# Optimization experiments

Hardware: AMD Instinct MI355X
Metric: run time of the kernel (lower is better)

## Reference

```python
import jax, jax.numpy as jnp
import numpy as np

MAX_LEN, BATCH, EMB = 512, 32, 41
HID, UNITS = 800, 20
BOND_LENS = jnp.array([1.329, 1.459, 1.525], jnp.float32)
BOND_ANGLES = jnp.array([2.034, 2.119, 1.937], jnp.float32)
INIT_ABC = jnp.array([[0.0, 0.0, 1.0], [0.0, 1.0, 0.0], [1.0, 0.0, 0.0]], jnp.float32)


def _lstm_dir(x, w_ih, w_hh, b, reverse):
    # x: [T, B, in]; returns hidden states [T, B, H]
    T, B, _ = x.shape
    H = w_hh.shape[1]
    xs = jnp.flip(x, 0) if reverse else x
    xw = jnp.einsum('tbi,gi->tbg', xs, w_ih) + b  # precompute input projection

    def step(carry, xt):
        h, c = carry
        gates = xt + h @ w_hh.T
        i, f, g, o = jnp.split(gates, 4, axis=-1)
        c = jax.nn.sigmoid(f) * c + jax.nn.sigmoid(i) * jnp.tanh(g)
        h = jax.nn.sigmoid(o) * jnp.tanh(c)
        return (h, c), h

    init = (jnp.zeros((B, H), x.dtype), jnp.zeros((B, H), x.dtype))
    _, hs = jax.lax.scan(step, init, xw)
    return jnp.flip(hs, 0) if reverse else hs


def _bilstm_layer(x, w_ih, w_hh, b):
    # w_ih: [2, 4H, in]; w_hh: [2, 4H, H]; b: [2, 4H]
    fwd = _lstm_dir(x, w_ih[0], w_hh[0], b[0], False)
    bwd = _lstm_dir(x, w_ih[1], w_hh[1], b[1], True)
    return jnp.concatenate([fwd, bwd], axis=-1)


def _geometric_unit(coords3, triplet):
    # coords3: [3, B, 3] last three atoms; triplet: [B, 3] torsion angles
    A, Bc, C = coords3[0], coords3[1], coords3[2]
    new = []
    for i in range(3):
        Tang, R, P = BOND_ANGLES[i], BOND_LENS[i], triplet[:, i]
        D2 = jnp.stack([-R * jnp.cos(Tang) * jnp.ones_like(P),
                        R * jnp.cos(P) * jnp.sin(Tang),
                        R * jnp.sin(P) * jnp.sin(Tang)], axis=1)  # [B,3]
        BC = C - Bc
        bc = BC / jnp.linalg.norm(BC, axis=1, keepdims=True)
        AB = Bc - A
        N = jnp.cross(AB, bc)
        n = N / jnp.linalg.norm(N, axis=1, keepdims=True)
        M = jnp.stack([bc, jnp.cross(n, bc), n], axis=2)  # [B,3,3]
        D = jnp.einsum('bij,bj->bi', M, D2) + C
        A, Bc, C = Bc, C, D
        new.append(D)
    return jnp.stack([A, Bc, C]), jnp.stack(new)  # carry, [3,B,3]


def setup_inputs() -> dict:
    key = jax.random.key(0)
    ks = jax.random.split(key, 10)
    k = 1.0 / np.sqrt(HID)
    u = lambda kk, shp, lim: jax.random.uniform(kk, shp, jnp.float32, -lim, lim)
    in0, in1 = EMB + 1, 2 * HID
    return {
        'sequences': jax.random.normal(ks[0], (MAX_LEN, BATCH, EMB), jnp.float32),
        'lengths': jnp.full((BATCH,), MAX_LEN, jnp.int64 if jax.config.jax_enable_x64 else jnp.int32),
        'w_ih0': u(ks[1], (2, 4 * HID, in0), k),
        'w_hh0': u(ks[2], (2, 4 * HID, HID), k),
        'b0': u(ks[3], (2, 4 * HID), k),
        'w_ih1': u(ks[4], (2, 4 * HID, in1), k),
        'w_hh1': u(ks[5], (2, 4 * HID, HID), k),
        'b1': u(ks[6], (2, 4 * HID), k),
        'lin_w': u(ks[7], (UNITS, 2 * HID), 1.0 / np.sqrt(2 * HID)),
        'lin_b': u(ks[8], (UNITS,), 1.0 / np.sqrt(2 * HID)),
        'alphabet': jax.random.uniform(ks[9], (UNITS, 3), jnp.float32, -3.14, 3.14),
    }


def reference(sequences, lengths, w_ih0, w_hh0, b0, w_ih1, w_hh1, b1, lin_w, lin_b, alphabet):
    T, B, _ = sequences.shape
    abs_pos = jnp.broadcast_to(jnp.arange(T, dtype=sequences.dtype)[:, None, None], (T, B, 1))
    x = jnp.concatenate([sequences, abs_pos], axis=2)  # [T, B, EMB+1]
    # 2-layer bidirectional LSTM (all lengths == max_len -> packing is identity)
    h = _bilstm_layer(x, w_ih0, w_hh0, b0)
    h = _bilstm_layer(h, w_ih1, w_hh1, b1)  # [T, B, 2H]
    # linear -> softmax over alphabet, trig angle decode
    soft = jax.nn.softmax(h @ lin_w.T + lin_b, axis=2)  # [T, B, UNITS]
    sine = soft @ jnp.sin(alphabet)   # [T, B, 3]
    cosine = soft @ jnp.cos(alphabet)
    out = jnp.arctan2(sine, cosine)   # torsion angle triplets
    # sequential geometric coordinate recurrence over timesteps 1..T-1
    init = jnp.broadcast_to(INIT_ABC[:, None, :], (3, B, 3))
    _, new_coords = jax.lax.scan(_geometric_unit, init, out[1:])  # [T-1, 3, B, 3]
    pred_coords = jnp.concatenate([init, new_coords.reshape(-1, B, 3)], axis=0)
    return pred_coords  # [3 + 3*(T-1), B, 3]
```

## Files before the change

kernel.cpp:

```cpp
#include <hip/hip_runtime.h>
#include <math.h>

#define T_LEN 512
#define NB    32
#define EMB_  41
#define IN0_  42
#define HID_  800
#define G4_   3200
#define IN1_  1600
#define NU    20
#define NCH   100

typedef unsigned short u16;
typedef unsigned int   u32;
typedef unsigned long long u64;
typedef __attribute__((ext_vector_type(8))) short short8;
typedef __attribute__((ext_vector_type(4))) float f32x4;

__device__ __forceinline__ float bf2f(u16 v) {
    union { u32 u; float f; } c; c.u = ((u32)v) << 16; return c.f;
}
__device__ __forceinline__ u16 f2bf(float f) {
    union { float f; u32 u; } c; c.f = f;
    u32 r = (c.u + 0x7fffu + ((c.u >> 16) & 1u)) >> 16;
    return (u16)r;
}
__device__ __forceinline__ short cvt_hl(float v, int hl) {
    u16 hi = f2bf(v);
    return hl ? (short)f2bf(v - bf2f(hi)) : (short)hi;
}
__device__ __forceinline__ f32x4 mfma16(short8 a, short8 b, f32x4 c) {
    return __builtin_amdgcn_mfma_f32_16x16x32_bf16(a, b, c, 0, 0, 0);
}
__device__ __forceinline__ void astore(u64* p, u64 v) {
    __hip_atomic_store(p, v, __ATOMIC_RELAXED, __HIP_MEMORY_SCOPE_AGENT);
}
__device__ __forceinline__ int afload(const int* p) {
    return __hip_atomic_load(p, __ATOMIC_RELAXED, __HIP_MEMORY_SCOPE_AGENT);
}
__device__ __forceinline__ void afstore(int* p, int v) {
    __hip_atomic_store(p, v, __ATOMIC_RELAXED, __HIP_MEMORY_SCOPE_AGENT);
}


__global__ __launch_bounds__(256, 1)
void lstm0_persist(const float* __restrict__ seq, const float* __restrict__ wih0,
                   const float* __restrict__ whh0, const float* __restrict__ bias,
                   u16* __restrict__ h0f, int* __restrict__ flags)
{
    __shared__ __align__(16) float part[2048];
    __shared__ __align__(16) u16 stageB[25600];
    __shared__ __align__(16) float w0l[32*48];
    __shared__ __align__(16) float xsl[32*48];
    __shared__ u16 hpk[NB*8];
    const int tid = threadIdx.x;
    const int d = blockIdx.x / NCH, ch = blockIdx.x % NCH;
    const int w = tid >> 6, l = tid & 63;
    const int p = w & 1, hl = w >> 1;
    int* myflags = flags + d*128;

    short8 wreg[25];
    {
        const int m = l & 15, g = p*2 + (m>>3), j = ch*8 + (m&7);
        const float* base = whh0 + ((size_t)(d*G4_ + g*HID_ + j))*HID_ + (l>>4)*8;
#pragma unroll
        for (int kc = 0; kc < 25; ++kc) {
            float4 f0 = *(const float4*)(base + kc*32);
            float4 f1 = *(const float4*)(base + kc*32 + 4);
            short8 v;
            v[0]=cvt_hl(f0.x,hl); v[1]=cvt_hl(f0.y,hl); v[2]=cvt_hl(f0.z,hl); v[3]=cvt_hl(f0.w,hl);
            v[4]=cvt_hl(f1.x,hl); v[5]=cvt_hl(f1.y,hl); v[6]=cvt_hl(f1.z,hl); v[7]=cvt_hl(f1.w,hl);
            wreg[kc] = v;
        }
    }
    for (int idx = tid; idx < 32*EMB_; idx += 256) {
        int r = idx / EMB_, k = idx % EMB_;
        int ju_ = r >> 2, g = r & 3;
        w0l[r*48 + k] = wih0[((size_t)(d*G4_ + g*HID_ + ch*8 + ju_))*IN0_ + k];
    }
    const int ju = tid >> 5, b = tid & 31;
    const int j = ch*8 + ju;
    const int nt = b >> 4, n = b & 15;
    float biasr[4], wpos[4];
#pragma unroll
    for (int g = 0; g < 4; ++g) {
        biasr[g] = bias[d*G4_ + g*HID_ + j];
        wpos[g]  = wih0[((size_t)(d*G4_ + g*HID_ + j))*IN0_ + EMB_];
    }
    float creg = 0.f;
    __syncthreads();

    for (int s = 0; s < T_LEN; ++s) {
        const int t = d ? (T_LEN-1-s) : s;

        for (int idx = tid; idx < 32*EMB_; idx += 256)
            xsl[(idx/EMB_)*48 + idx%EMB_] = seq[(size_t)t*(NB*EMB_) + idx];

        if (s > 0 && tid < NCH)
            while (afload(myflags + tid) < s) __builtin_amdgcn_s_sleep(1);
        __syncthreads();

        if (s == 0) {
#pragma unroll
            for (int q = 0; q < 25; ++q) ((u64*)stageB)[tid + q*256] = 0ull;
        } else {
            const int tprev = d ? (T_LEN - s) : (s - 1);
            const u64* src = (const u64*)(h0f + (size_t)tprev*51200) + d*6400;
            u64 tmp[25];
#pragma unroll
            for (int q = 0; q < 25; ++q) tmp[q] = src[tid + q*256];
#pragma unroll
            for (int q = 0; q < 25; ++q) ((u64*)stageB)[tid + q*256] = tmp[q];
        }
        __syncthreads();

        f32x4 acc0 = {0.f,0.f,0.f,0.f}, acc1 = {0.f,0.f,0.f,0.f};
#pragma unroll 5
        for (int kc = 0; kc < 25; ++kc) {
            short8 b0 = *(const short8*)(stageB + kc*1024 + l*8);
            short8 b1 = *(const short8*)(stageB + kc*1024 + 512 + l*8);
            acc0 = mfma16(wreg[kc], b0, acc0);
            acc1 = mfma16(wreg[kc], b1, acc1);
        }
        {
            const int mrow = (l>>4)*4, nn = l & 15;
#pragma unroll
            for (int r = 0; r < 4; ++r) {
                part[(((p*2+hl)*2 + 0)*16 + mrow + r)*16 + nn] = acc0[r];
                part[(((p*2+hl)*2 + 1)*16 + mrow + r)*16 + nn] = acc1[r];
            }
        }
        __syncthreads();

        float dot0 = 0.f, dot1 = 0.f, dot2 = 0.f, dot3 = 0.f;
        {
            const float* wr = &w0l[ju*4*48];
            const float* xr = &xsl[b*48];
#pragma unroll
            for (int k4 = 0; k4 < 40; k4 += 4) {
                float4 xk = *(const float4*)(xr + k4);
                float4 w0 = *(const float4*)(wr + 0*48 + k4);
                float4 w1 = *(const float4*)(wr + 1*48 + k4);
                float4 w2 = *(const float4*)(wr + 2*48 + k4);
                float4 w3 = *(const float4*)(wr + 3*48 + k4);
                dot0 += w0.x*xk.x + w0.y*xk.y + w0.z*xk.z + w0.w*xk.w;
                dot1 += w1.x*xk.x + w1.y*xk.y + w1.z*xk.z + w1.w*xk.w;
                dot2 += w2.x*xk.x + w2.y*xk.y + w2.z*xk.z + w2.w*xk.w;
                dot3 += w3.x*xk.x + w3.y*xk.y + w3.z*xk.z + w3.w*xk.w;
            }
            float xk = xr[40];
            dot0 += wr[0*48+40]*xk; dot1 += wr[1*48+40]*xk;
            dot2 += wr[2*48+40]*xk; dot3 += wr[3*48+40]*xk;
        }
        float v[4] = {dot0, dot1, dot2, dot3};
#pragma unroll
        for (int g = 0; g < 4; ++g) {
            const int pp = g >> 1, m = (g & 1)*8 + ju;
            v[g] += part[(((pp*2+0)*2 + nt)*16 + m)*16 + n]
                  + part[(((pp*2+1)*2 + nt)*16 + m)*16 + n]
                  + biasr[g] + (float)t * wpos[g];
        }
        float ig = 1.f/(1.f + expf(-v[0]));
        float fg = 1.f/(1.f + expf(-v[1]));
        float gg = tanhf(v[2]);
        float og = 1.f/(1.f + expf(-v[3]));
        creg = fg * creg + ig * gg;
        hpk[b*8 + ju] = f2bf(og * tanhf(creg));
        __syncthreads();

        if (tid < 64) {
            const int bb = tid >> 1, half = tid & 1;
            const u16* hp = &hpk[bb*8 + half*4];
            u64 pk = (u64)hp[0] | ((u64)hp[1]<<16) | ((u64)hp[2]<<32) | ((u64)hp[3]<<48);
            const int ntb = bb >> 4, llb = ((ch&3)<<4) | (bb&15);
            const int xoff = ((d*25 + (ch>>2))*2 + ntb)*128 + llb*2 + half;
            astore((u64*)(h0f + (size_t)t*51200) + xoff, pk);
        }
        __syncthreads();
        if (tid == 0) afstore(myflags + ch, s+1);
    }
}

__global__ __launch_bounds__(256, 1)
void lstm1_persist(const float* __restrict__ wih1, const float* __restrict__ whh1,
                   const float* __restrict__ bias, const float* __restrict__ lin_w,
                   const u16* __restrict__ h0f, u16* __restrict__ h1f,
                   int* __restrict__ flags, float* __restrict__ logits)
{
    __shared__ __align__(16) u16 wihL[2*50*512];
    __shared__ __align__(16) u16 stageB[25600];
    __shared__ __align__(16) float part[2048];
    __shared__ u16 hpk[NB*8];
    const int tid = threadIdx.x;
    const int d = blockIdx.x / NCH, ch = blockIdx.x % NCH;
    const int w = tid >> 6, l = tid & 63;
    const int p = w & 1, hl = w >> 1;
    int* myflags = flags + d*128;

    short8 wreg[25];
    {
        const int m = l & 15, g = p*2 + (m>>3), j = ch*8 + (m&7);
        const float* base = whh1 + ((size_t)(d*G4_ + g*HID_ + j))*HID_ + (l>>4)*8;
#pragma unroll
        for (int kc = 0; kc < 25; ++kc) {
            float4 f0 = *(const float4*)(base + kc*32);
            float4 f1 = *(const float4*)(base + kc*32 + 4);
            short8 v;
            v[0]=cvt_hl(f0.x,hl); v[1]=cvt_hl(f0.y,hl); v[2]=cvt_hl(f0.z,hl); v[3]=cvt_hl(f0.w,hl);
            v[4]=cvt_hl(f1.x,hl); v[5]=cvt_hl(f1.y,hl); v[6]=cvt_hl(f1.z,hl); v[7]=cvt_hl(f1.w,hl);
            wreg[kc] = v;
        }
    }
    for (int o = tid; o < 6400; o += 256) {
        int pp = o / 3200, r = o % 3200, kc = r >> 6, ll = r & 63;
        int m = ll & 15, g = pp*2 + (m>>3), jj = ch*8 + (m&7);
        const float* base = wih1 + ((size_t)(d*G4_ + g*HID_ + jj))*IN1_ + kc*32 + (ll>>4)*8;
        float4 f0 = *(const float4*)base;
        float4 f1 = *(const float4*)(base + 4);
        short8 v;
        v[0]=(short)f2bf(f0.x); v[1]=(short)f2bf(f0.y); v[2]=(short)f2bf(f0.z); v[3]=(short)f2bf(f0.w);
        v[4]=(short)f2bf(f1.x); v[5]=(short)f2bf(f1.y); v[6]=(short)f2bf(f1.z); v[7]=(short)f2bf(f1.w);
        *(short8*)&wihL[o*8] = v;
    }
    const int ol = tid >> 5, ln = tid & 31;
    const int lo = ch*7 + ol;
    const bool lown = (ol < 7) && (lo < NB*NU);
    int lofs = 0;
    float wlin[25];
    if (lown) {
        const int bb = lo / NU, uu = lo % NU;
        lofs = (bb >> 4)*512 + ((((ln >> 3) << 4) | (bb & 15)))*8 + (ln & 7);
        const float* wrow = lin_w + (size_t)uu*IN1_ + d*HID_ + ln;
#pragma unroll
        for (int i = 0; i < 25; ++i) wlin[i] = wrow[i*32];
    }
    const int ju = tid >> 5, b = tid & 31;
    const int j = ch*8 + ju;
    const int nt = b >> 4, n = b & 15;
    float biasr[4];
#pragma unroll
    for (int g = 0; g < 4; ++g) biasr[g] = bias[d*G4_ + g*HID_ + j];
    float creg = 0.f;
    __syncthreads();

    for (int s = 0; s < T_LEN; ++s) {
        const int t = d ? (T_LEN-1-s) : s;

        f32x4 acc0 = {0.f,0.f,0.f,0.f}, acc1 = {0.f,0.f,0.f,0.f};
        {
            const u16* xb = h0f + (size_t)t*51200;
#pragma unroll 5
            for (int kc = 0; kc < 25; ++kc) {
                const int idx = hl*25 + kc;
                short8 a  = *(const short8*)&wihL[(p*50 + idx)*512 + l*8];
                short8 b0 = *(const short8*)(xb + idx*1024 + l*8);
                short8 b1 = *(const short8*)(xb + idx*1024 + 512 + l*8);
                acc0 = mfma16(a, b0, acc0);
                acc1 = mfma16(a, b1, acc1);
            }
        }

        if (s > 0 && tid < NCH)
            while (afload(myflags + tid) < s) __builtin_amdgcn_s_sleep(1);
        __syncthreads();

        if (s == 0) {
#pragma unroll
            for (int q = 0; q < 25; ++q) ((u64*)stageB)[tid + q*256] = 0ull;
        } else {
            const int tprev = d ? (T_LEN - s) : (s - 1);
            const u64* src = (const u64*)(h1f + (size_t)tprev*51200) + d*6400;
            u64 tmp[25];
#pragma unroll
            for (int q = 0; q < 25; ++q) tmp[q] = src[tid + q*256];
#pragma unroll
            for (int q = 0; q < 25; ++q) ((u64*)stageB)[tid + q*256] = tmp[q];
        }
        __syncthreads();

#pragma unroll 5
        for (int kc = 0; kc < 25; ++kc) {
            short8 b0 = *(const short8*)(stageB + kc*1024 + l*8);
            short8 b1 = *(const short8*)(stageB + kc*1024 + 512 + l*8);
            acc0 = mfma16(wreg[kc], b0, acc0);
            acc1 = mfma16(wreg[kc], b1, acc1);
        }
        {
            const int mrow = (l>>4)*4, nn = l & 15;
#pragma unroll
            for (int r = 0; r < 4; ++r) {
                part[(((p*2+hl)*2 + 0)*16 + mrow + r)*16 + nn] = acc0[r];
                part[(((p*2+hl)*2 + 1)*16 + mrow + r)*16 + nn] = acc1[r];
            }
        }
        __syncthreads();

        float v[4];
#pragma unroll
        for (int g = 0; g < 4; ++g) {
            const int pp = g >> 1, m = (g & 1)*8 + ju;
            v[g] = part[(((pp*2+0)*2 + nt)*16 + m)*16 + n]
                 + part[(((pp*2+1)*2 + nt)*16 + m)*16 + n] + biasr[g];
        }
        float ig = 1.f/(1.f + expf(-v[0]));
        float fg = 1.f/(1.f + expf(-v[1]));
        float gg = tanhf(v[2]);
        float og = 1.f/(1.f + expf(-v[3]));
        creg = fg * creg + ig * gg;
        float hn = og * tanhf(creg);
        hpk[b*8 + ju] = f2bf(hn);
        __syncthreads();

        if (tid < 64) {
            const int bb = tid >> 1, half = tid & 1;
            const u16* hp = &hpk[bb*8 + half*4];
            u64 pk = (u64)hp[0] | ((u64)hp[1]<<16) | ((u64)hp[2]<<32) | ((u64)hp[3]<<48);
            const int ntb = bb >> 4, llb = ((ch&3)<<4) | (bb&15);
            const int xoff = ((d*25 + (ch>>2))*2 + ntb)*128 + llb*2 + half;
            astore((u64*)(h1f + (size_t)t*51200) + xoff, pk);
        }
        __syncthreads();
        if (tid == 0) afstore(myflags + ch, s+1);

        if (s > 0 && lown) {
            float sum = 0.f;
#pragma unroll
            for (int i = 0; i < 25; ++i)
                sum += bf2f(stageB[i*1024 + lofs]) * wlin[i];
#pragma unroll
            for (int off2 = 16; off2; off2 >>= 1) sum += __shfl_down(sum, off2, 32);
            if (ln == 0) {
                const int tprev = d ? (T_LEN - s) : (s - 1);
                logits[((size_t)d*T_LEN + tprev)*640 + lo] = sum;
            }
        }
    }
    if (tid < NCH)
        while (afload(myflags + tid) < T_LEN) __builtin_amdgcn_s_sleep(1);
    __syncthreads();
    {
        const int tlast = d ? 0 : (T_LEN - 1);
        const u64* src = (const u64*)(h1f + (size_t)tlast*51200) + d*6400;
        u64 tmp[25];
#pragma unroll
        for (int q = 0; q < 25; ++q) tmp[q] = src[tid + q*256];
#pragma unroll
        for (int q = 0; q < 25; ++q) ((u64*)stageB)[tid + q*256] = tmp[q];
    }
    __syncthreads();
    if (lown) {
        float sum = 0.f;
#pragma unroll
        for (int i = 0; i < 25; ++i)
            sum += bf2f(stageB[i*1024 + lofs]) * wlin[i];
#pragma unroll
        for (int off2 = 16; off2; off2 >>= 1) sum += __shfl_down(sum, off2, 32);
        if (ln == 0) {
            const int tprev = d ? 0 : (T_LEN - 1);
            logits[((size_t)d*T_LEN + tprev)*640 + lo] = sum;
        }
    }
}

__global__ __launch_bounds__(256)
void epilogue(const float* __restrict__ logits, const float* __restrict__ lin_b,
              const float* __restrict__ alphabet, float* __restrict__ cs)
{
    __shared__ float sa[NU*3], ca[NU*3], lb[NU];
    const int tid = threadIdx.x;
    if (tid < NU*3) { float al = alphabet[tid]; sa[tid] = sinf(al); ca[tid] = cosf(al); }
    if (tid < NU) lb[tid] = lin_b[tid];
    __syncthreads();
    const int row = blockIdx.x*256 + tid;
    if (row >= T_LEN*NB) return;
    const int t = row >> 5, b = row & 31;
    float lg[NU];
    float m = -1e30f;
#pragma unroll 4
    for (int u = 0; u < NU; ++u) {
        lg[u] = lb[u] + logits[(size_t)t*640 + b*NU + u]
                      + logits[((size_t)T_LEN + t)*640 + b*NU + u];
        m = fmaxf(m, lg[u]);
    }
    float ssum = 0.f;
#pragma unroll 4
    for (int u = 0; u < NU; ++u) { lg[u] = expf(lg[u] - m); ssum += lg[u]; }
    float inv = 1.f / ssum;
#pragma unroll
    for (int i = 0; i < 3; ++i) {
        float sv = 0.f, cv = 0.f;
#pragma unroll 4
        for (int u = 0; u < NU; ++u) {
            float sw = lg[u] * inv;
            sv += sw * sa[u*3 + i];
            cv += sw * ca[u*3 + i];
        }
        float rinv = rsqrtf(fmaxf(sv*sv + cv*cv, 1e-30f));
        *(float2*)(cs + ((size_t)row*3 + i)*2) = make_float2(cv*rinv, sv*rinv);
    }
}

__global__ __launch_bounds__(64)
void geometry(const float* __restrict__ cs, float* __restrict__ out)
{
    const int b = threadIdx.x;
    if (b >= NB) return;
    const float blen[3] = {1.329f, 1.459f, 1.525f};
    const float bang[3] = {2.034f, 2.119f, 1.937f};
    float sT[3], cT[3];
#pragma unroll
    for (int i = 0; i < 3; ++i) { sT[i] = sinf(bang[i]); cT[i] = cosf(bang[i]); }

    float Ax=0.f,Ay=0.f,Az=1.f, Bx=0.f,By=1.f,Bz=0.f, Cx=1.f,Cy=0.f,Cz=0.f;
    out[(0*NB + b)*3 + 0] = 0.f; out[(0*NB + b)*3 + 1] = 0.f; out[(0*NB + b)*3 + 2] = 1.f;
    out[(1*NB + b)*3 + 0] = 0.f; out[(1*NB + b)*3 + 1] = 1.f; out[(1*NB + b)*3 + 2] = 0.f;
    out[(2*NB + b)*3 + 0] = 1.f; out[(2*NB + b)*3 + 1] = 0.f; out[(2*NB + b)*3 + 2] = 0.f;

    for (int t = 1; t < T_LEN; ++t) {
        float2 pc[3];
#pragma unroll
        for (int i = 0; i < 3; ++i)
            pc[i] = *(const float2*)(cs + (((size_t)t*NB + b)*3 + i)*2);
#pragma unroll
        for (int i = 0; i < 3; ++i) {
            float R = blen[i];
            float d2x = -R*cT[i], d2y = R*pc[i].x*sT[i], d2z = R*pc[i].y*sT[i];
            float bcx = Cx-Bx, bcy = Cy-By, bcz = Cz-Bz;
            float inv = rsqrtf(bcx*bcx + bcy*bcy + bcz*bcz);
            bcx *= inv; bcy *= inv; bcz *= inv;
            float abx = Bx-Ax, aby = By-Ay, abz = Bz-Az;
            float nx = aby*bcz - abz*bcy;
            float ny = abz*bcx - abx*bcz;
            float nz = abx*bcy - aby*bcx;
            inv = rsqrtf(fmaxf(nx*nx + ny*ny + nz*nz, 1e-30f));
            nx *= inv; ny *= inv; nz *= inv;
            float mx = ny*bcz - nz*bcy;
            float my = nz*bcx - nx*bcz;
            float mz = nx*bcy - ny*bcx;
            float Dx = bcx*d2x + mx*d2y + nx*d2z + Cx;
            float Dy = bcy*d2x + my*d2y + ny*d2z + Cy;
            float Dz = bcz*d2x + mz*d2y + nz*d2z + Cz;
            Ax=Bx; Ay=By; Az=Bz; Bx=Cx; By=Cy; Bz=Cz; Cx=Dx; Cy=Dy; Cz=Dz;
            const int r = 3 + (t-1)*3 + i;
            out[((size_t)r*NB + b)*3 + 0] = Dx;
            out[((size_t)r*NB + b)*3 + 1] = Dy;
            out[((size_t)r*NB + b)*3 + 2] = Dz;
        }
    }
}

extern "C" void kernel_launch(void* const* d_in, const int* in_sizes, int n_in,
                              void* d_out, int out_size, void* d_ws, size_t ws_size,
                              hipStream_t stream)
{
    (void)in_sizes; (void)n_in; (void)out_size; (void)ws_size;
    const float* seq   = (const float*)d_in[0];
    const float* w_ih0 = (const float*)d_in[2];
    const float* w_hh0 = (const float*)d_in[3];
    const float* b0    = (const float*)d_in[4];
    const float* w_ih1 = (const float*)d_in[5];
    const float* w_hh1 = (const float*)d_in[6];
    const float* b1    = (const float*)d_in[7];
    const float* lin_w = (const float*)d_in[8];
    const float* lin_b = (const float*)d_in[9];
    const float* alpha = (const float*)d_in[10];

    char* ws = (char*)d_ws;
    size_t off = 0;
    u16* h0f   = (u16*)(ws + off); off += 52428800ull;
    u16* h1f   = (u16*)(ws + off); off += 52428800ull;
    int* flagsL0 = (int*)(ws + off); off += 1024ull;
    int* flagsL1 = (int*)(ws + off); off += 1024ull;
    float* logits = (float*)(ws + off); off += 2621440ull;
    float* cs = (float*)(ws + off); off += 393216ull;

    hipMemsetAsync(flagsL0, 0, 2048, stream);

    lstm0_persist<<<dim3(2*NCH), dim3(256), 0, stream>>>(seq, w_ih0, w_hh0, b0, h0f, flagsL0);

    lstm1_persist<<<dim3(2*NCH), dim3(256), 0, stream>>>(w_ih1, w_hh1, b1, lin_w, h0f, h1f,
                                                         flagsL1, logits);

    epilogue<<<dim3(64), dim3(256), 0, stream>>>(logits, lin_b, alpha, cs);
    geometry<<<dim3(1), dim3(64), 0, stream>>>(cs, (float*)d_out);
}
```

Before: 9.387 ms.

## Read hidden state directly from global memory and cut per-step barriers in persistent LSTMs

Each wave now polls the cross-block step flags itself with a wave-wide vote, instead of one thread group spinning followed by a block barrier. The hidden-state vector is loaded straight from global memory into the MFMA operands, no longer staged through LDS with an extra barrier. The flag store is issued by wave 0 after a vmcnt wait rather than after a block-wide barrier, and the input slice buffer is double-buffered to avoid a write-after-read hazard. This shortens the serial critical path of each timestep, at the cost of redundant global and L2 reads per wave and weaker ordering guarantees on the relaxed atomics.

```diff
diff --git a/kernel.cpp b/kernel.cpp
--- a/kernel.cpp
+++ b/kernel.cpp
@@ -49,9 +49,8 @@
                    u16* __restrict__ h0f, int* __restrict__ flags)
 {
     __shared__ __align__(16) float part[2048];
-    __shared__ __align__(16) u16 stageB[25600];
     __shared__ __align__(16) float w0l[32*48];
-    __shared__ __align__(16) float xsl[32*48];
+    __shared__ __align__(16) float xsl[2][32*48];
     __shared__ u16 hpk[NB*8];
     const int tid = threadIdx.x;
     const int d = blockIdx.x / NCH, ch = blockIdx.x % NCH;
@@ -88,39 +87,34 @@
         wpos[g]  = wih0[((size_t)(d*G4_ + g*HID_ + j))*IN0_ + EMB_];
     }
     float creg = 0.f;
+    const int pi1 = l, pi2 = (l + 64 < NCH) ? (l + 64) : l;
     __syncthreads();
 
     for (int s = 0; s < T_LEN; ++s) {
         const int t = d ? (T_LEN-1-s) : s;
 
         for (int idx = tid; idx < 32*EMB_; idx += 256)
-            xsl[(idx/EMB_)*48 + idx%EMB_] = seq[(size_t)t*(NB*EMB_) + idx];
-
-        if (s > 0 && tid < NCH)
-            while (afload(myflags + tid) < s) __builtin_amdgcn_s_sleep(1);
-        __syncthreads();
-
-        if (s == 0) {
-#pragma unroll
-            for (int q = 0; q < 25; ++q) ((u64*)stageB)[tid + q*256] = 0ull;
-        } else {
+            xsl[s&1][(idx/EMB_)*48 + idx%EMB_] = seq[(size_t)t*(NB*EMB_) + idx];
+
+        if (s > 0) {
+            for (;;) {
+                bool ok = (afload(myflags + pi1) >= s) && (afload(myflags + pi2) >= s);
+                if (__all(ok)) break;
+                __builtin_amdgcn_s_sleep(1);
+            }
+        }
+
+        f32x4 acc0 = {0.f,0.f,0.f,0.f}, acc1 = {0.f,0.f,0.f,0.f};
+        if (s > 0) {
             const int tprev = d ? (T_LEN - s) : (s - 1);
-            const u64* src = (const u64*)(h0f + (size_t)tprev*51200) + d*6400;
-            u64 tmp[25];
-#pragma unroll
-            for (int q = 0; q < 25; ++q) tmp[q] = src[tid + q*256];
-#pragma unroll
-            for (int q = 0; q < 25; ++q) ((u64*)stageB)[tid + q*256] = tmp[q];
-        }
-        __syncthreads();
-
-        f32x4 acc0 = {0.f,0.f,0.f,0.f}, acc1 = {0.f,0.f,0.f,0.f};
+            const u16* hb = h0f + (size_t)tprev*51200 + d*25600;
 #pragma unroll 5
-        for (int kc = 0; kc < 25; ++kc) {
-            short8 b0 = *(const short8*)(stageB + kc*1024 + l*8);
-            short8 b1 = *(const short8*)(stageB + kc*1024 + 512 + l*8);
-            acc0 = mfma16(wreg[kc], b0, acc0);
-            acc1 = mfma16(wreg[kc], b1, acc1);
+            for (int kc = 0; kc < 25; ++kc) {
+                short8 b0 = *(const short8*)(hb + kc*1024 + l*8);
+                short8 b1 = *(const short8*)(hb + kc*1024 + 512 + l*8);
+                acc0 = mfma16(wreg[kc], b0, acc0);
+                acc1 = mfma16(wreg[kc], b1, acc1);
+            }
         }
         {
             const int mrow = (l>>4)*4, nn = l & 15;
@@ -135,7 +129,7 @@
         float dot0 = 0.f, dot1 = 0.f, dot2 = 0.f, dot3 = 0.f;
         {
             const float* wr = &w0l[ju*4*48];
-            const float* xr = &xsl[b*48];
+            const float* xr = &xsl[s&1][b*48];
 #pragma unroll
             for (int k4 = 0; k4 < 40; k4 += 4) {
                 float4 xk = *(const float4*)(xr + k4);
@@ -168,16 +162,16 @@
         hpk[b*8 + ju] = f2bf(og * tanhf(creg));
         __syncthreads();
 
-        if (tid < 64) {
-            const int bb = tid >> 1, half = tid & 1;
+        if (w == 0) {
+            const int bb = l >> 1, half = l & 1;
             const u16* hp = &hpk[bb*8 + half*4];
             u64 pk = (u64)hp[0] | ((u64)hp[1]<<16) | ((u64)hp[2]<<32) | ((u64)hp[3]<<48);
             const int ntb = bb >> 4, llb = ((ch&3)<<4) | (bb&15);
             const int xoff = ((d*25 + (ch>>2))*2 + ntb)*128 + llb*2 + half;
             astore((u64*)(h0f + (size_t)t*51200) + xoff, pk);
-        }
-        __syncthreads();
-        if (tid == 0) afstore(myflags + ch, s+1);
+            asm volatile("s_waitcnt vmcnt(0)" ::: "memory");
+            if (l == 0) afstore(myflags + ch, s+1);
+        }
     }
 }
 
@@ -188,7 +182,6 @@
                    int* __restrict__ flags, float* __restrict__ logits)
 {
     __shared__ __align__(16) u16 wihL[2*50*512];
-    __shared__ __align__(16) u16 stageB[25600];
     __shared__ __align__(16) float part[2048];
     __shared__ u16 hpk[NB*8];
     const int tid = threadIdx.x;
@@ -241,6 +234,7 @@
 #pragma unroll
     for (int g = 0; g < 4; ++g) biasr[g] = bias[d*G4_ + g*HID_ + j];
     float creg = 0.f;
+    const int pi1 = l, pi2 = (l + 64 < NCH) ? (l + 64) : l;
     __syncthreads();
 
     for (int s = 0; s < T_LEN; ++s) {
@@ -260,30 +254,24 @@
             }
         }
 
-        if (s > 0 && tid < NCH)
-            while (afload(myflags + tid) < s) __builtin_amdgcn_s_sleep(1);
-        __syncthreads();
-
-        if (s == 0) {
-#pragma unroll
-            for (int q = 0; q < 25; ++q) ((u64*)stageB)[tid + q*256] = 0ull;
-        } else {
+        if (s > 0) {
+            for (;;) {
+                bool ok = (afload(myflags + pi1) >= s) && (afload(myflags + pi2) >= s);
+                if (__all(ok)) break;
+                __builtin_amdgcn_s_sleep(1);
+            }
+        }
+
+        if (s > 0) {
             const int tprev = d ? (T_LEN - s) : (s - 1);
-            const u64* src = (const u64*)(h1f + (size_t)tprev*51200) + d*6400;
-            u64 tmp[25];
-#pragma unroll
-            for (int q = 0; q < 25; ++q) tmp[q] = src[tid + q*256];
-#pragma unroll
-            for (int q = 0; q < 25; ++q) ((u64*)stageB)[tid + q*256] = tmp[q];
-        }
-        __syncthreads();
-
+            const u16* hb = h1f + (size_t)tprev*51200 + d*25600;
 #pragma unroll 5
-        for (int kc = 0; kc < 25; ++kc) {
-            short8 b0 = *(const short8*)(stageB + kc*1024 + l*8);
-            short8 b1 = *(const short8*)(stageB + kc*1024 + 512 + l*8);
-            acc0 = mfma16(wreg[kc], b0, acc0);
-            acc1 = mfma16(wreg[kc], b1, acc1);
+            for (int kc = 0; kc < 25; ++kc) {
+                short8 b0 = *(const short8*)(hb + kc*1024 + l*8);
+                short8 b1 = *(const short8*)(hb + kc*1024 + 512 + l*8);
+                acc0 = mfma16(wreg[kc], b0, acc0);
+                acc1 = mfma16(wreg[kc], b1, acc1);
+            }
         }
         {
             const int mrow = (l>>4)*4, nn = l & 15;
@@ -311,53 +299,49 @@
         hpk[b*8 + ju] = f2bf(hn);
         __syncthreads();
 
-        if (tid < 64) {
-            const int bb = tid >> 1, half = tid & 1;
+        if (w == 0) {
+            const int bb = l >> 1, half = l & 1;
             const u16* hp = &hpk[bb*8 + half*4];
             u64 pk = (u64)hp[0] | ((u64)hp[1]<<16) | ((u64)hp[2]<<32) | ((u64)hp[3]<<48);
             const int ntb = bb >> 4, llb = ((ch&3)<<4) | (bb&15);
             const int xoff = ((d*25 + (ch>>2))*2 + ntb)*128 + llb*2 + half;
             astore((u64*)(h1f + (size_t)t*51200) + xoff, pk);
-        }
-        __syncthreads();
-        if (tid == 0) afstore(myflags + ch, s+1);
+            asm volatile("s_waitcnt vmcnt(0)" ::: "memory");
+            if (l == 0) afstore(myflags + ch, s+1);
+        }
 
         if (s > 0 && lown) {
+            const int tprev = d ? (T_LEN - s) : (s - 1);
+            const u16* hb = h1f + (size_t)tprev*51200 + d*25600;
             float sum = 0.f;
 #pragma unroll
             for (int i = 0; i < 25; ++i)
-                sum += bf2f(stageB[i*1024 + lofs]) * wlin[i];
+                sum += bf2f(hb[i*1024 + lofs]) * wlin[i];
+#pragma unroll
+            for (int off2 = 16; off2; off2 >>= 1) sum += __shfl_down(sum, off2, 32);
+            if (ln == 0)
+                logits[((size_t)d*T_LEN + tprev)*640 + lo] = sum;
+        }
+    }
+    {
+        for (;;) {
+            bool ok = (afload(myflags + pi1) >= T_LEN) && (afload(myflags + pi2) >= T_LEN);
+            if (__all(ok)) break;
+            __builtin_amdgcn_s_sleep(1);
+        }
+        if (lown) {
+            const int tlast = d ? 0 : (T_LEN - 1);
+            const u16* hb = h1f + (size_t)tlast*51200 + d*25600;
+            float sum = 0.f;
+#pragma unroll
+            for (int i = 0; i < 25; ++i)
+                sum += bf2f(hb[i*1024 + lofs]) * wlin[i];
 #pragma unroll
             for (int off2 = 16; off2; off2 >>= 1) sum += __shfl_down(sum, off2, 32);
             if (ln == 0) {
-                const int tprev = d ? (T_LEN - s) : (s - 1);
+                const int tprev = d ? 0 : (T_LEN - 1);
                 logits[((size_t)d*T_LEN + tprev)*640 + lo] = sum;
             }
-        }
-    }
-    if (tid < NCH)
-        while (afload(myflags + tid) < T_LEN) __builtin_amdgcn_s_sleep(1);
-    __syncthreads();
-    {
-        const int tlast = d ? 0 : (T_LEN - 1);
-        const u64* src = (const u64*)(h1f + (size_t)tlast*51200) + d*6400;
-        u64 tmp[25];
-#pragma unroll
-        for (int q = 0; q < 25; ++q) tmp[q] = src[tid + q*256];
-#pragma unroll
-        for (int q = 0; q < 25; ++q) ((u64*)stageB)[tid + q*256] = tmp[q];
-    }
-    __syncthreads();
-    if (lown) {
-        float sum = 0.f;
-#pragma unroll
-        for (int i = 0; i < 25; ++i)
-            sum += bf2f(stageB[i*1024 + lofs]) * wlin[i];
-#pragma unroll
-        for (int off2 = 16; off2; off2 >>= 1) sum += __shfl_down(sum, off2, 32);
-        if (ln == 0) {
-            const int tprev = d ? 0 : (T_LEN - 1);
-            logits[((size_t)d*T_LEN + tprev)*640 + lo] = sum;
         }
     }
 }
```

Result: slower. 10.87 ms (+15.8%).

## Add producer warps to precompute input projections one step ahead in LSTM kernels

Applied to the files above, without the earlier changes.

Both persistent LSTM kernels now launch 512 threads: the first 256 do the recurrent MFMA and gate math, and the extra 256 act as producers. The producers compute the next timestep's input projection (layer 0: the embedding dot plus bias and position term; layer 1: the h0 x W_ih MFMA from weights held in registers instead of LDS) into a double-buffered shared array. This takes the input projection off the serial critical path of each step and frees the large W_ih LDS buffer in layer 1. In exchange, every step has more threads at each barrier, and register pressure is higher at 512 threads per block.

```diff
diff --git a/kernel.cpp b/kernel.cpp
--- a/kernel.cpp
+++ b/kernel.cpp
@@ -43,7 +43,7 @@
 }
 
 
-__global__ __launch_bounds__(256, 1)
+__global__ __launch_bounds__(512, 1)
 void lstm0_persist(const float* __restrict__ seq, const float* __restrict__ wih0,
                    const float* __restrict__ whh0, const float* __restrict__ bias,
                    u16* __restrict__ h0f, int* __restrict__ flags)
@@ -51,16 +51,21 @@
     __shared__ __align__(16) float part[2048];
     __shared__ __align__(16) u16 stageB[25600];
     __shared__ __align__(16) float w0l[32*48];
-    __shared__ __align__(16) float xsl[32*48];
+    __shared__ __align__(16) float xsl[2][32*48];
+    __shared__ __align__(16) float xw0[2][1024];
     __shared__ u16 hpk[NB*8];
     const int tid = threadIdx.x;
     const int d = blockIdx.x / NCH, ch = blockIdx.x % NCH;
+    const bool comp = tid < 256;
     const int w = tid >> 6, l = tid & 63;
     const int p = w & 1, hl = w >> 1;
+    const int xt = tid & 255;
+    const int xju = xt >> 5, xb = xt & 31;
     int* myflags = flags + d*128;
 
     short8 wreg[25];
-    {
+    float biasr[4], wpos[4];
+    if (comp) {
         const int m = l & 15, g = p*2 + (m>>3), j = ch*8 + (m&7);
         const float* base = whh0 + ((size_t)(d*G4_ + g*HID_ + j))*HID_ + (l>>4)*8;
 #pragma unroll
@@ -72,57 +77,112 @@
             v[4]=cvt_hl(f1.x,hl); v[5]=cvt_hl(f1.y,hl); v[6]=cvt_hl(f1.z,hl); v[7]=cvt_hl(f1.w,hl);
             wreg[kc] = v;
         }
-    }
-    for (int idx = tid; idx < 32*EMB_; idx += 256) {
-        int r = idx / EMB_, k = idx % EMB_;
-        int ju_ = r >> 2, g = r & 3;
-        w0l[r*48 + k] = wih0[((size_t)(d*G4_ + g*HID_ + ch*8 + ju_))*IN0_ + k];
+    } else {
+        for (int idx = xt; idx < 32*EMB_; idx += 256) {
+            int r = idx / EMB_, k = idx % EMB_;
+            int ju_ = r >> 2, g = r & 3;
+            w0l[r*48 + k] = wih0[((size_t)(d*G4_ + g*HID_ + ch*8 + ju_))*IN0_ + k];
+        }
+#pragma unroll
+        for (int g = 0; g < 4; ++g) {
+            biasr[g] = bias[d*G4_ + g*HID_ + ch*8 + xju];
+            wpos[g]  = wih0[((size_t)(d*G4_ + g*HID_ + ch*8 + xju))*IN0_ + EMB_];
+        }
+        const int t0 = d ? (T_LEN-1) : 0;
+        const int t1 = d ? (T_LEN-2) : 1;
+        for (int idx = xt; idx < 32*EMB_; idx += 256) {
+            xsl[0][(idx/EMB_)*48 + idx%EMB_] = seq[(size_t)t0*(NB*EMB_) + idx];
+            xsl[1][(idx/EMB_)*48 + idx%EMB_] = seq[(size_t)t1*(NB*EMB_) + idx];
+        }
     }
     const int ju = tid >> 5, b = tid & 31;
-    const int j = ch*8 + ju;
     const int nt = b >> 4, n = b & 15;
-    float biasr[4], wpos[4];
-#pragma unroll
-    for (int g = 0; g < 4; ++g) {
-        biasr[g] = bias[d*G4_ + g*HID_ + j];
-        wpos[g]  = wih0[((size_t)(d*G4_ + g*HID_ + j))*IN0_ + EMB_];
-    }
     float creg = 0.f;
     __syncthreads();
 
+    if (!comp) {
+        const int t0 = d ? (T_LEN-1) : 0;
+        const float* wr = &w0l[xju*4*48];
+        const float* xr = &xsl[0][xb*48];
+        float dt[4] = {0.f,0.f,0.f,0.f};
+#pragma unroll
+        for (int k4 = 0; k4 < 40; k4 += 4) {
+            float4 xk = *(const float4*)(xr + k4);
+#pragma unroll
+            for (int g = 0; g < 4; ++g) {
+                float4 wv = *(const float4*)(wr + g*48 + k4);
+                dt[g] += wv.x*xk.x + wv.y*xk.y + wv.z*xk.z + wv.w*xk.w;
+            }
+        }
+        float xk = xr[40];
+#pragma unroll
+        for (int g = 0; g < 4; ++g) dt[g] += wr[g*48+40]*xk;
+        *(float4*)&xw0[0][(xju*32+xb)*4] = make_float4(
+            dt[0]+biasr[0]+(float)t0*wpos[0], dt[1]+biasr[1]+(float)t0*wpos[1],
+            dt[2]+biasr[2]+(float)t0*wpos[2], dt[3]+biasr[3]+(float)t0*wpos[3]);
+    }
+
     for (int s = 0; s < T_LEN; ++s) {
         const int t = d ? (T_LEN-1-s) : s;
-
-        for (int idx = tid; idx < 32*EMB_; idx += 256)
-            xsl[(idx/EMB_)*48 + idx%EMB_] = seq[(size_t)t*(NB*EMB_) + idx];
-
-        if (s > 0 && tid < NCH)
-            while (afload(myflags + tid) < s) __builtin_amdgcn_s_sleep(1);
-        __syncthreads();
-
-        if (s == 0) {
-#pragma unroll
-            for (int q = 0; q < 25; ++q) ((u64*)stageB)[tid + q*256] = 0ull;
+        if (comp) {
+            if (s > 0 && tid < NCH)
+                while (afload(myflags + tid) < s) __builtin_amdgcn_s_sleep(1);
         } else {
-            const int tprev = d ? (T_LEN - s) : (s - 1);
-            const u64* src = (const u64*)(h0f + (size_t)tprev*51200) + d*6400;
-            u64 tmp[25];
-#pragma unroll
-            for (int q = 0; q < 25; ++q) tmp[q] = src[tid + q*256];
-#pragma unroll
-            for (int q = 0; q < 25; ++q) ((u64*)stageB)[tid + q*256] = tmp[q];
-        }
-        __syncthreads();
-
-        f32x4 acc0 = {0.f,0.f,0.f,0.f}, acc1 = {0.f,0.f,0.f,0.f};
+            const int sx = s + 1;
+            if (sx < T_LEN) {
+                const int tx = d ? (T_LEN-1-sx) : sx;
+                const float* wr = &w0l[xju*4*48];
+                const float* xr = &xsl[sx&1][xb*48];
+                float dt[4] = {0.f,0.f,0.f,0.f};
+#pragma unroll
+                for (int k4 = 0; k4 < 40; k4 += 4) {
+                    float4 xk = *(const float4*)(xr + k4);
+#pragma unroll
+                    for (int g = 0; g < 4; ++g) {
+                        float4 wv = *(const float4*)(wr + g*48 + k4);
+                        dt[g] += wv.x*xk.x + wv.y*xk.y + wv.z*xk.z + wv.w*xk.w;
+                    }
+                }
+                float xk = xr[40];
+#pragma unroll
+                for (int g = 0; g < 4; ++g) dt[g] += wr[g*48+40]*xk;
+                *(float4*)&xw0[sx&1][(xju*32+xb)*4] = make_float4(
+                    dt[0]+biasr[0]+(float)tx*wpos[0], dt[1]+biasr[1]+(float)tx*wpos[1],
+                    dt[2]+biasr[2]+(float)tx*wpos[2], dt[3]+biasr[3]+(float)tx*wpos[3]);
+            }
+            if (s + 2 < T_LEN) {
+                const int t2 = d ? (T_LEN-1-(s+2)) : (s+2);
+                for (int idx = xt; idx < 32*EMB_; idx += 256)
+                    xsl[s&1][(idx/EMB_)*48 + idx%EMB_] = seq[(size_t)t2*(NB*EMB_) + idx];
+            }
+        }
+        __syncthreads();
+
+        if (comp) {
+            if (s == 0) {
+#pragma unroll
+                for (int q = 0; q < 25; ++q) ((u64*)stageB)[tid + q*256] = 0ull;
+            } else {
+                const int tprev = d ? (T_LEN - s) : (s - 1);
+                const u64* src = (const u64*)(h0f + (size_t)tprev*51200) + d*6400;
+                u64 tmp[25];
+#pragma unroll
+                for (int q = 0; q < 25; ++q) tmp[q] = src[tid + q*256];
+#pragma unroll
+                for (int q = 0; q < 25; ++q) ((u64*)stageB)[tid + q*256] = tmp[q];
+            }
+        }
+        __syncthreads();
+
+        if (comp) {
+            f32x4 acc0 = {0.f,0.f,0.f,0.f}, acc1 = {0.f,0.f,0.f,0.f};
 #pragma unroll 5
-        for (int kc = 0; kc < 25; ++kc) {
-            short8 b0 = *(const short8*)(stageB + kc*1024 + l*8);
-            short8 b1 = *(const short8*)(stageB + kc*1024 + 512 + l*8);
-            acc0 = mfma16(wreg[kc], b0, acc0);
-            acc1 = mfma16(wreg[kc], b1, acc1);
-        }
-        {
+            for (int kc = 0; kc < 25; ++kc) {
+                short8 b0 = *(const short8*)(stageB + kc*1024 + l*8);
+                short8 b1 = *(const short8*)(stageB + kc*1024 + 512 + l*8);
+                acc0 = mfma16(wreg[kc], b0, acc0);
+                acc1 = mfma16(wreg[kc], b1, acc1);
+            }
             const int mrow = (l>>4)*4, nn = l & 15;
 #pragma unroll
             for (int r = 0; r < 4; ++r) {
@@ -132,43 +192,26 @@
         }
         __syncthreads();
 
-        float dot0 = 0.f, dot1 = 0.f, dot2 = 0.f, dot3 = 0.f;
-        {
-            const float* wr = &w0l[ju*4*48];
-            const float* xr = &xsl[b*48];
-#pragma unroll
-            for (int k4 = 0; k4 < 40; k4 += 4) {
-                float4 xk = *(const float4*)(xr + k4);
-                float4 w0 = *(const float4*)(wr + 0*48 + k4);
-                float4 w1 = *(const float4*)(wr + 1*48 + k4);
-                float4 w2 = *(const float4*)(wr + 2*48 + k4);
-                float4 w3 = *(const float4*)(wr + 3*48 + k4);
-                dot0 += w0.x*xk.x + w0.y*xk.y + w0.z*xk.z + w0.w*xk.w;
-                dot1 += w1.x*xk.x + w1.y*xk.y + w1.z*xk.z + w1.w*xk.w;
-                dot2 += w2.x*xk.x + w2.y*xk.y + w2.z*xk.z + w2.w*xk.w;
-                dot3 += w3.x*xk.x + w3.y*xk.y + w3.z*xk.z + w3.w*xk.w;
-            }
-            float xk = xr[40];
-            dot0 += wr[0*48+40]*xk; dot1 += wr[1*48+40]*xk;
-            dot2 += wr[2*48+40]*xk; dot3 += wr[3*48+40]*xk;
-        }
-        float v[4] = {dot0, dot1, dot2, dot3};
-#pragma unroll
-        for (int g = 0; g < 4; ++g) {
-            const int pp = g >> 1, m = (g & 1)*8 + ju;
-            v[g] += part[(((pp*2+0)*2 + nt)*16 + m)*16 + n]
-                  + part[(((pp*2+1)*2 + nt)*16 + m)*16 + n]
-                  + biasr[g] + (float)t * wpos[g];
-        }
-        float ig = 1.f/(1.f + expf(-v[0]));
-        float fg = 1.f/(1.f + expf(-v[1]));
-        float gg = tanhf(v[2]);
-        float og = 1.f/(1.f + expf(-v[3]));
-        creg = fg * creg + ig * gg;
-        hpk[b*8 + ju] = f2bf(og * tanhf(creg));
-        __syncthreads();
-
-        if (tid < 64) {
+        if (comp) {
+            float4 xwv = *(const float4*)&xw0[s&1][(ju*32+b)*4];
+            float xv[4] = {xwv.x, xwv.y, xwv.z, xwv.w};
+            float v[4];
+#pragma unroll
+            for (int g = 0; g < 4; ++g) {
+                const int pp = g >> 1, m = (g & 1)*8 + ju;
+                v[g] = part[(((pp*2+0)*2 + nt)*16 + m)*16 + n]
+                     + part[(((pp*2+1)*2 + nt)*16 + m)*16 + n] + xv[g];
+            }
+            float ig = 1.f/(1.f + expf(-v[0]));
+            float fg = 1.f/(1.f + expf(-v[1]));
+            float gg = tanhf(v[2]);
+            float og = 1.f/(1.f + expf(-v[3]));
+            creg = fg * creg + ig * gg;
+            hpk[b*8 + ju] = f2bf(og * tanhf(creg));
+        }
+        __syncthreads();
+
+        if (comp && tid < 64) {
             const int bb = tid >> 1, half = tid & 1;
             const u16* hp = &hpk[bb*8 + half*4];
             u64 pk = (u64)hp[0] | ((u64)hp[1]<<16) | ((u64)hp[2]<<32) | ((u64)hp[3]<<48);
@@ -181,24 +224,28 @@
     }
 }
 
-__global__ __launch_bounds__(256, 1)
+__global__ __launch_bounds__(512, 1)
 void lstm1_persist(const float* __restrict__ wih1, const float* __restrict__ whh1,
                    const float* __restrict__ bias, const float* __restrict__ lin_w,
                    const u16* __restrict__ h0f, u16* __restrict__ h1f,
                    int* __restrict__ flags, float* __restrict__ logits)
 {
-    __shared__ __align__(16) u16 wihL[2*50*512];
     __shared__ __align__(16) u16 stageB[25600];
     __shared__ __align__(16) float part[2048];
+    __shared__ __align__(16) float xw1[2][2048];
     __shared__ u16 hpk[NB*8];
     const int tid = threadIdx.x;
     const int d = blockIdx.x / NCH, ch = blockIdx.x % NCH;
+    const bool comp = tid < 256;
     const int w = tid >> 6, l = tid & 63;
     const int p = w & 1, hl = w >> 1;
+    const int xt = tid & 255;
+    const int xw_ = xt >> 6, xl = xt & 63;
+    const int xp = xw_ & 1, xhl = xw_ >> 1;
     int* myflags = flags + d*128;
 
     short8 wreg[25];
-    {
+    if (comp) {
         const int m = l & 15, g = p*2 + (m>>3), j = ch*8 + (m&7);
         const float* base = whh1 + ((size_t)(d*G4_ + g*HID_ + j))*HID_ + (l>>4)*8;
 #pragma unroll
@@ -210,21 +257,23 @@
             v[4]=cvt_hl(f1.x,hl); v[5]=cvt_hl(f1.y,hl); v[6]=cvt_hl(f1.z,hl); v[7]=cvt_hl(f1.w,hl);
             wreg[kc] = v;
         }
-    }
-    for (int o = tid; o < 6400; o += 256) {
-        int pp = o / 3200, r = o % 3200, kc = r >> 6, ll = r & 63;
-        int m = ll & 15, g = pp*2 + (m>>3), jj = ch*8 + (m&7);
-        const float* base = wih1 + ((size_t)(d*G4_ + g*HID_ + jj))*IN1_ + kc*32 + (ll>>4)*8;
-        float4 f0 = *(const float4*)base;
-        float4 f1 = *(const float4*)(base + 4);
-        short8 v;
-        v[0]=(short)f2bf(f0.x); v[1]=(short)f2bf(f0.y); v[2]=(short)f2bf(f0.z); v[3]=(short)f2bf(f0.w);
-        v[4]=(short)f2bf(f1.x); v[5]=(short)f2bf(f1.y); v[6]=(short)f2bf(f1.z); v[7]=(short)f2bf(f1.w);
-        *(short8*)&wihL[o*8] = v;
+    } else {
+        const int m = xl & 15, g = xp*2 + (m>>3), jj = ch*8 + (m&7);
+#pragma unroll
+        for (int kc = 0; kc < 25; ++kc) {
+            const int idx = xhl*25 + kc;
+            const float* base = wih1 + ((size_t)(d*G4_ + g*HID_ + jj))*IN1_ + idx*32 + (xl>>4)*8;
+            float4 f0 = *(const float4*)base;
+            float4 f1 = *(const float4*)(base + 4);
+            short8 v;
+            v[0]=(short)f2bf(f0.x); v[1]=(short)f2bf(f0.y); v[2]=(short)f2bf(f0.z); v[3]=(short)f2bf(f0.w);
+            v[4]=(short)f2bf(f1.x); v[5]=(short)f2bf(f1.y); v[6]=(short)f2bf(f1.z); v[7]=(short)f2bf(f1.w);
+            wreg[kc] = v;
+        }
     }
     const int ol = tid >> 5, ln = tid & 31;
     const int lo = ch*7 + ol;
-    const bool lown = (ol < 7) && (lo < NB*NU);
+    const bool lown = comp && (ol < 7) && (lo < NB*NU);
     int lofs = 0;
     float wlin[25];
     if (lown) {
@@ -238,54 +287,87 @@
     const int j = ch*8 + ju;
     const int nt = b >> 4, n = b & 15;
     float biasr[4];
-#pragma unroll
-    for (int g = 0; g < 4; ++g) biasr[g] = bias[d*G4_ + g*HID_ + j];
+    if (comp) {
+#pragma unroll
+        for (int g = 0; g < 4; ++g) biasr[g] = bias[d*G4_ + g*HID_ + j];
+    }
     float creg = 0.f;
-    __syncthreads();
+
+    if (!comp) {
+        const int t1 = d ? (T_LEN-1) : 0;
+        const u16* xb0 = h0f + (size_t)t1*51200;
+        f32x4 a0 = {0.f,0.f,0.f,0.f}, a1 = {0.f,0.f,0.f,0.f};
+#pragma unroll 5
+        for (int kc = 0; kc < 25; ++kc) {
+            const int idx = xhl*25 + kc;
+            short8 b0 = *(const short8*)(xb0 + idx*1024 + xl*8);
+            short8 b1 = *(const short8*)(xb0 + idx*1024 + 512 + xl*8);
+            a0 = mfma16(wreg[kc], b0, a0);
+            a1 = mfma16(wreg[kc], b1, a1);
+        }
+#pragma unroll
+        for (int r = 0; r < 4; ++r) {
+            xw1[0][((xp*2+xhl)*2 + 0)*256 + xl*4 + r] = a0[r];
+            xw1[0][((xp*2+xhl)*2 + 1)*256 + xl*4 + r] = a1[r];
+        }
+    }
 
     for (int s = 0; s < T_LEN; ++s) {
         const int t = d ? (T_LEN-1-s) : s;
-
-        f32x4 acc0 = {0.f,0.f,0.f,0.f}, acc1 = {0.f,0.f,0.f,0.f};
-        {
-            const u16* xb = h0f + (size_t)t*51200;
+        if (comp) {
+            if (s > 0 && tid < NCH)
+                while (afload(myflags + tid) < s) __builtin_amdgcn_s_sleep(1);
+        } else if (s + 1 < T_LEN) {
+            const int sx = s + 1;
+            const int t1 = d ? (T_LEN-1-sx) : sx;
+            const u16* xb0 = h0f + (size_t)t1*51200;
+            f32x4 a0 = {0.f,0.f,0.f,0.f}, a1 = {0.f,0.f,0.f,0.f};
 #pragma unroll 5
             for (int kc = 0; kc < 25; ++kc) {
-                const int idx = hl*25 + kc;
-                short8 a  = *(const short8*)&wihL[(p*50 + idx)*512 + l*8];
-                short8 b0 = *(const short8*)(xb + idx*1024 + l*8);
-                short8 b1 = *(const short8*)(xb + idx*1024 + 512 + l*8);
-                acc0 = mfma16(a, b0, acc0);
-                acc1 = mfma16(a, b1, acc1);
-            }
-        }
-
-        if (s > 0 && tid < NCH)
-            while (afload(myflags + tid) < s) __builtin_amdgcn_s_sleep(1);
-        __syncthreads();
-
-        if (s == 0) {
-#pragma unroll
-            for (int q = 0; q < 25; ++q) ((u64*)stageB)[tid + q*256] = 0ull;
-        } else {
-            const int tprev = d ? (T_LEN - s) : (s - 1);
-            const u64* src = (const u64*)(h1f + (size_t)tprev*51200) + d*6400;
-            u64 tmp[25];
-#pragma unroll
-            for (int q = 0; q < 25; ++q) tmp[q] = src[tid + q*256];
-#pragma unroll
-            for (int q = 0; q < 25; ++q) ((u64*)stageB)[tid + q*256] = tmp[q];
-        }
-        __syncthreads();
-
+                const int idx = xhl*25 + kc;
+                short8 b0 = *(const short8*)(xb0 + idx*1024 + xl*8);
+                short8 b1 = *(const short8*)(xb0 + idx*1024 + 512 + xl*8);
+                a0 = mfma16(wreg[kc], b0, a0);
+                a1 = mfma16(wreg[kc], b1, a1);
+            }
+#pragma unroll
+            for (int r = 0; r < 4; ++r) {
+                xw1[sx&1][((xp*2+xhl)*2 + 0)*256 + xl*4 + r] = a0[r];
+                xw1[sx&1][((xp*2+xhl)*2 + 1)*256 + xl*4 + r] = a1[r];
+            }
+        }
+        __syncthreads();
+
+        if (comp) {
+            if (s == 0) {
+#pragma unroll
+                for (int q = 0; q < 25; ++q) ((u64*)stageB)[tid + q*256] = 0ull;
+            } else {
+                const int tprev = d ? (T_LEN - s) : (s - 1);
+                const u64* src = (const u64*)(h1f + (size_t)tprev*51200) + d*6400;
+                u64 tmp[25];
+#pragma unroll
+                for (int q = 0; q < 25; ++q) tmp[q] = src[tid + q*256];
+#pragma unroll
+                for (int q = 0; q < 25; ++q) ((u64*)stageB)[tid + q*256] = tmp[q];
+            }
+        }
+        __syncthreads();
+
+        if (comp) {
+            f32x4 acc0, acc1;
+#pragma unroll
+            for (int r = 0; r < 4; ++r) {
+                acc0[r] = xw1[s&1][((p*2+hl)*2 + 0)*256 + l*4 + r];
+                acc1[r] = xw1[s&1][((p*2+hl)*2 + 1)*256 + l*4 + r];
+            }
 #pragma unroll 5
-        for (int kc = 0; kc < 25; ++kc) {
-            short8 b0 = *(const short8*)(stageB + kc*1024 + l*8);
-            short8 b1 = *(const short8*)(stageB + kc*1024 + 512 + l*8);
-            acc0 = mfma16(wreg[kc], b0, acc0);
-            acc1 = mfma16(wreg[kc], b1, acc1);
-        }
-        {
+            for (int kc = 0; kc < 25; ++kc) {
+                short8 b0 = *(const short8*)(stageB + kc*1024 + l*8);
+                short8 b1 = *(const short8*)(stageB + kc*1024 + 512 + l*8);
+                acc0 = mfma16(wreg[kc], b0, acc0);
+                acc1 = mfma16(wreg[kc], b1, acc1);
+            }
             const int mrow = (l>>4)*4, nn = l & 15;
 #pragma unroll
             for (int r = 0; r < 4; ++r) {
@@ -295,23 +377,24 @@
         }
         __syncthreads();
 
-        float v[4];
-#pragma unroll
-        for (int g = 0; g < 4; ++g) {
-            const int pp = g >> 1, m = (g & 1)*8 + ju;
-            v[g] = part[(((pp*2+0)*2 + nt)*16 + m)*16 + n]
-                 + part[(((pp*2+1)*2 + nt)*16 + m)*16 + n] + biasr[g];
-        }
-        float ig = 1.f/(1.f + expf(-v[0]));
-        float fg = 1.f/(1.f + expf(-v[1]));
-        float gg = tanhf(v[2]);
-        float og = 1.f/(1.f + expf(-v[3]));
-        creg = fg * creg + ig * gg;
-        float hn = og * tanhf(creg);
-        hpk[b*8 + ju] = f2bf(hn);
-        __syncthreads();
-
-        if (tid < 64) {
+        if (comp) {
+            float v[4];
+#pragma unroll
+            for (int g = 0; g < 4; ++g) {
+                const int pp = g >> 1, m = (g & 1)*8 + ju;
+                v[g] = part[(((pp*2+0)*2 + nt)*16 + m)*16 + n]
+                     + part[(((pp*2+1)*2 + nt)*16 + m)*16 + n] + biasr[g];
+            }
+            float ig = 1.f/(1.f + expf(-v[0]));
+            float fg = 1.f/(1.f + expf(-v[1]));
+            float gg = tanhf(v[2]);
+            float og = 1.f/(1.f + expf(-v[3]));
+            creg = fg * creg + ig * gg;
+            hpk[b*8 + ju] = f2bf(og * tanhf(creg));
+        }
+        __syncthreads();
+
+        if (comp && tid < 64) {
             const int bb = tid >> 1, half = tid & 1;
             const u16* hp = &hpk[bb*8 + half*4];
             u64 pk = (u64)hp[0] | ((u64)hp[1]<<16) | ((u64)hp[2]<<32) | ((u64)hp[3]<<48);
@@ -338,7 +421,7 @@
     if (tid < NCH)
         while (afload(myflags + tid) < T_LEN) __builtin_amdgcn_s_sleep(1);
     __syncthreads();
-    {
+    if (comp) {
         const int tlast = d ? 0 : (T_LEN - 1);
         const u64* src = (const u64*)(h1f + (size_t)tlast*51200) + d*6400;
         u64 tmp[25];
@@ -476,9 +559,9 @@
 
     hipMemsetAsync(flagsL0, 0, 2048, stream);
 
-    lstm0_persist<<<dim3(2*NCH), dim3(256), 0, stream>>>(seq, w_ih0, w_hh0, b0, h0f, flagsL0);
-
-    lstm1_persist<<<dim3(2*NCH), dim3(256), 0, stream>>>(w_ih1, w_hh1, b1, lin_w, h0f, h1f,
+    lstm0_persist<<<dim3(2*NCH), dim3(512), 0, stream>>>(seq, w_ih0, w_hh0, b0, h0f, flagsL0);
+
+    lstm1_persist<<<dim3(2*NCH), dim3(512), 0, stream>>>(w_ih1, w_hh1, b1, lin_w, h0f, h1f,
                                                          flagsL1, logits);
 
     epilogue<<<dim3(64), dim3(256), 0, stream>>>(logits, lin_b, alpha, cs);
```

Result: slower. 12.52 ms (+33.4%).
